# Performance work log

Measured on AMD Instinct MI355X. Metric: run time of the kernel, lower is better.

The kernel has to match this reference:

```python
import jax, jax.numpy as jnp
import numpy as np

C = 256  # num_channels
N = 524288  # number of 2D query points


def _linear_params(key, fan_in, fan_out):
    # torch nn.Linear default init: U(-1/sqrt(fan_in), 1/sqrt(fan_in))
    kw, kb = jax.random.split(key)
    bound = 1.0 / np.sqrt(fan_in)
    W = jax.random.uniform(kw, (fan_in, fan_out), jnp.float32, -bound, bound)
    b = jax.random.uniform(kb, (fan_out,), jnp.float32, -bound, bound)
    return W, b


def setup_inputs() -> dict:
    key = jax.random.key(0)
    k_uv, k0, k1, k2, k3 = jax.random.split(key, 5)
    uv = jax.random.uniform(k_uv, (N, 2), jnp.float32)
    W_in, b_in = _linear_params(k0, 4, C)
    W_h0, b_h0 = _linear_params(k1, C, C)
    W_h1, b_h1 = _linear_params(k2, C, C)
    W_out, b_out = _linear_params(k3, C, 3)
    return {
        "uv": uv,
        "W_in": W_in, "b_in": b_in,
        "W_h0": W_h0, "b_h0": b_h0,
        "W_h1": W_h1, "b_h1": b_h1,
        "W_out": W_out, "b_out": b_out,
    }


def reference(uv, W_in, b_in, W_h0, b_h0, W_h1, b_h1, W_out, b_out):
    # NOTE: in the original, `encoded = 2*pi*uv` is overwritten, so the
    # effective encoding is simply [cos(uv), sin(uv)] -> last dim 4.
    encoded = jnp.concatenate([jnp.cos(uv), jnp.sin(uv)], axis=-1)  # [N, 4]
    h = jax.nn.relu(encoded @ W_in + b_in)   # [N, C]
    h = jax.nn.relu(h @ W_h0 + b_h0)          # [N, C]
    h = jax.nn.relu(h @ W_h1 + b_h1)          # [N, C]
    out = jax.nn.sigmoid(h @ W_out + b_out)   # [N, 3]
    return out
```

## Files before the change

kernel.cpp:

```cpp
#include <hip/hip_runtime.h>
#include <hip/hip_bf16.h>
#include <math.h>

#define CCH 256
#define MT  64
#define ROWE 264
#define TPB 512

typedef __attribute__((ext_vector_type(8))) short short8;
typedef __attribute__((ext_vector_type(4))) float f32x4;
typedef __attribute__((ext_vector_type(2))) unsigned int uint2v;

__device__ unsigned short g_T0[CCH * CCH];
__device__ unsigned short g_T1[CCH * CCH];
__device__ unsigned short g_Wo[16 * CCH];

__device__ __forceinline__ unsigned short f2bf(float f) {
  unsigned u = __float_as_uint(f);
  u += 0x7fffu + ((u >> 16) & 1u);
  return (unsigned short)(u >> 16);
}
__device__ __forceinline__ unsigned cvtpk(float lo, float hi) {
  unsigned r;
  asm("v_cvt_pk_bf16_f32 %0, %1, %2" : "=v"(r) : "v"(lo), "v"(hi));
  return r;
}

__global__ void transpose_w(const float* __restrict__ W0,
                            const float* __restrict__ W1) {
  __shared__ float tile[32][33];
  const float* src = blockIdx.z ? W1 : W0;
  unsigned short* dst = blockIdx.z ? g_T1 : g_T0;
  const int tx = threadIdx.x, ty = threadIdx.y;
  const int k0 = blockIdx.y * 32, n0 = blockIdx.x * 32;
#pragma unroll
  for (int r = 0; r < 4; ++r)
    tile[ty + r * 8][tx] = src[(k0 + ty + r * 8) * CCH + n0 + tx];
  __syncthreads();
#pragma unroll
  for (int r = 0; r < 4; ++r) {
    const int n = n0 + ty + r * 8;
    dst[n * CCH + k0 + tx] = f2bf(tile[tx][ty + r * 8]);
  }
}

__global__ void prep_wo(const float* __restrict__ W_out) {
  const int k = threadIdx.x;
#pragma unroll
  for (int j = 0; j < 16; ++j)
    g_Wo[j * CCH + k] = (j < 3) ? f2bf(W_out[k * 3 + j]) : (unsigned short)0;
}

__device__ __forceinline__ void mfma_gemm(
    const unsigned short (*__restrict__ src)[ROWE],
    const unsigned short* __restrict__ Wt,
    f32x4 acc[4][2], int wv, int l16, int lk8) {
#pragma unroll
  for (int mt = 0; mt < 4; ++mt)
#pragma unroll
    for (int nt = 0; nt < 2; ++nt)
      acc[mt][nt] = (f32x4){0.f, 0.f, 0.f, 0.f};

  const unsigned short* w0p = &Wt[(wv * 32 + l16) * CCH + lk8 * 8];
  const unsigned short* w1p = w0p + 16 * CCH;
  const unsigned short* a0p = &src[l16][lk8 * 8];

#pragma unroll
  for (int kk = 0; kk < 8; ++kk) {
    const int k = kk * 32;
    const short8 w0 = *(const short8*)&w0p[k];
    const short8 w1 = *(const short8*)&w1p[k];
#pragma unroll
    for (int mt = 0; mt < 4; ++mt) {
      const short8 a = *(const short8*)&a0p[mt * 16 * ROWE + k];
      acc[mt][0] = __builtin_amdgcn_mfma_f32_16x16x32_bf16(w0, a, acc[mt][0], 0, 0, 0);
      acc[mt][1] = __builtin_amdgcn_mfma_f32_16x16x32_bf16(w1, a, acc[mt][1], 0, 0, 0);
    }
  }
}

__device__ __forceinline__ void epilogue_store(
    const f32x4 acc[4][2], unsigned short (*__restrict__ dst)[ROWE],
    const float* __restrict__ bias, int wv, int l16, int lk8) {
#pragma unroll
  for (int nt = 0; nt < 2; ++nt) {
    const int ch0 = wv * 32 + nt * 16 + lk8 * 4;
    const f32x4 bv = *(const f32x4*)&bias[ch0];
#pragma unroll
    for (int mt = 0; mt < 4; ++mt) {
      uint2v pk;
      pk[0] = cvtpk(fmaxf(acc[mt][nt][0] + bv[0], 0.f),
                    fmaxf(acc[mt][nt][1] + bv[1], 0.f));
      pk[1] = cvtpk(fmaxf(acc[mt][nt][2] + bv[2], 0.f),
                    fmaxf(acc[mt][nt][3] + bv[3], 0.f));
      *(uint2v*)&dst[mt * 16 + l16][ch0] = pk;
    }
  }
}

__global__ __launch_bounds__(TPB, 6) void nerf_fused(
    const float* __restrict__ uv,
    const float* __restrict__ W_in, const float* __restrict__ b_in,
    const float* __restrict__ b_h0, const float* __restrict__ b_h1,
    const float* __restrict__ b_out,
    float* __restrict__ out) {
  __shared__ unsigned short hA[MT][ROWE];

  const int tid = threadIdx.x;
  const long n0 = (long)blockIdx.x * MT;
  const int wv = tid >> 6, ln = tid & 63;
  const int l16 = ln & 15, lk8 = ln >> 4;

  {
    const int p = tid >> 3;
    const int t7 = tid & 7;
    const float u = uv[(n0 + p) * 2 + 0];
    const float v = uv[(n0 + p) * 2 + 1];
    const float e0 = __cosf(u), e1 = __cosf(v), e2 = __sinf(u), e3 = __sinf(v);
#pragma unroll
    for (int j = 0; j < 8; ++j) {
      const int c = t7 * 4 + j * 32;
      const f32x4 w0 = *(const f32x4*)&W_in[0 * CCH + c];
      const f32x4 w1 = *(const f32x4*)&W_in[1 * CCH + c];
      const f32x4 w2 = *(const f32x4*)&W_in[2 * CCH + c];
      const f32x4 w3 = *(const f32x4*)&W_in[3 * CCH + c];
      const f32x4 bb = *(const f32x4*)&b_in[c];
      float x[4];
#pragma unroll
      for (int i = 0; i < 4; ++i)
        x[i] = fmaxf(bb[i] + e0 * w0[i] + e1 * w1[i] + e2 * w2[i] + e3 * w3[i], 0.f);
      uint2v pk;
      pk[0] = cvtpk(x[0], x[1]);
      pk[1] = cvtpk(x[2], x[3]);
      *(uint2v*)&hA[p][c] = pk;
    }
  }
  __syncthreads();

  f32x4 acc[4][2];

  mfma_gemm(hA, g_T0, acc, wv, l16, lk8);
  __syncthreads();
  epilogue_store(acc, hA, b_h0, wv, l16, lk8);
  __syncthreads();

  mfma_gemm(hA, g_T1, acc, wv, l16, lk8);
  __syncthreads();
  epilogue_store(acc, hA, b_h1, wv, l16, lk8);
  __syncthreads();

  if (wv < 4) {
    f32x4 oacc = (f32x4){0.f, 0.f, 0.f, 0.f};
#pragma unroll
    for (int kk = 0; kk < 8; ++kk) {
      const int k = kk * 32 + lk8 * 8;
      const short8 wo = *(const short8*)&g_Wo[l16 * CCH + k];
      const short8 hb = *(const short8*)&hA[wv * 16 + l16][k];
      oacc = __builtin_amdgcn_mfma_f32_16x16x32_bf16(wo, hb, oacc, 0, 0, 0);
    }
    if (lk8 == 0) {
      const long pt = n0 + wv * 16 + l16;
#pragma unroll
      for (int i = 0; i < 3; ++i)
        out[pt * 3 + i] = 1.f / (1.f + __expf(-(oacc[i] + b_out[i])));
    }
  }
}

extern "C" void kernel_launch(void* const* d_in, const int* in_sizes, int n_in,
                              void* d_out, int out_size, void* d_ws, size_t ws_size,
                              hipStream_t stream) {
  const float* uv    = (const float*)d_in[0];
  const float* W_in  = (const float*)d_in[1];
  const float* b_in  = (const float*)d_in[2];
  const float* W_h0  = (const float*)d_in[3];
  const float* b_h0  = (const float*)d_in[4];
  const float* W_h1  = (const float*)d_in[5];
  const float* b_h1  = (const float*)d_in[6];
  const float* W_out = (const float*)d_in[7];
  const float* b_out = (const float*)d_in[8];

  const int N = in_sizes[0] / 2;

  transpose_w<<<dim3(8, 8, 2), dim3(32, 8), 0, stream>>>(W_h0, W_h1);
  prep_wo<<<1, CCH, 0, stream>>>(W_out);
  nerf_fused<<<dim3(N / MT), dim3(TPB), 0, stream>>>(
      uv, W_in, b_in, b_h0, b_h1, b_out, (float*)d_out);
}
```

Baseline: 417.9 us.

## Persistent kernel with LDS-resident weights and global h1 spill

Replaces the per-tile fused kernel with a persistent kernel of 256 blocks of 1024 threads, each handling 2048 points. Each weight matrix is loaded into LDS once per block, and the first layer's activations are computed in registers and fed straight into MFMA. The hidden state after layer 1 is spilled to a 256MB global bf16 buffer and re-read for layer 2, and the output layer becomes a scalar dot product with shuffle and LDS reduction. This removes the repeated global weight reads, but it adds a large round-trip of activations through global memory and a hardcoded N buffer, so the spill traffic may outweigh the weight reuse.

```diff
diff --git a/kernel.cpp b/kernel.cpp
--- a/kernel.cpp
+++ b/kernel.cpp
@@ -3,17 +3,23 @@
 #include <math.h>
 
 #define CCH 256
-#define MT  64
-#define ROWE 264
-#define TPB 512
+#define WROW 264
+#define TPB 1024
+#define NBLK 256
+#define PPB 2048
+#define PPI 256
+#define NITER 8
 
 typedef __attribute__((ext_vector_type(8))) short short8;
 typedef __attribute__((ext_vector_type(4))) float f32x4;
+typedef __attribute__((ext_vector_type(2))) float f32x2;
+typedef __attribute__((ext_vector_type(4))) unsigned int uint4v;
 typedef __attribute__((ext_vector_type(2))) unsigned int uint2v;
 
 __device__ unsigned short g_T0[CCH * CCH];
 __device__ unsigned short g_T1[CCH * CCH];
-__device__ unsigned short g_Wo[16 * CCH];
+__device__ float g_Wof[4 * CCH];
+__device__ unsigned short g_h1[(size_t)524288 * CCH];
 
 __device__ __forceinline__ unsigned short f2bf(float f) {
   unsigned u = __float_as_uint(f);
@@ -44,126 +50,180 @@
   }
 }
 
-__global__ void prep_wo(const float* __restrict__ W_out) {
+__global__ void prep_wof(const float* __restrict__ W_out) {
   const int k = threadIdx.x;
 #pragma unroll
-  for (int j = 0; j < 16; ++j)
-    g_Wo[j * CCH + k] = (j < 3) ? f2bf(W_out[k * 3 + j]) : (unsigned short)0;
-}
-
-__device__ __forceinline__ void mfma_gemm(
-    const unsigned short (*__restrict__ src)[ROWE],
-    const unsigned short* __restrict__ Wt,
-    f32x4 acc[4][2], int wv, int l16, int lk8) {
-#pragma unroll
-  for (int mt = 0; mt < 4; ++mt)
-#pragma unroll
-    for (int nt = 0; nt < 2; ++nt)
-      acc[mt][nt] = (f32x4){0.f, 0.f, 0.f, 0.f};
-
-  const unsigned short* w0p = &Wt[(wv * 32 + l16) * CCH + lk8 * 8];
-  const unsigned short* w1p = w0p + 16 * CCH;
-  const unsigned short* a0p = &src[l16][lk8 * 8];
-
-#pragma unroll
-  for (int kk = 0; kk < 8; ++kk) {
-    const int k = kk * 32;
-    const short8 w0 = *(const short8*)&w0p[k];
-    const short8 w1 = *(const short8*)&w1p[k];
-#pragma unroll
-    for (int mt = 0; mt < 4; ++mt) {
-      const short8 a = *(const short8*)&a0p[mt * 16 * ROWE + k];
-      acc[mt][0] = __builtin_amdgcn_mfma_f32_16x16x32_bf16(w0, a, acc[mt][0], 0, 0, 0);
-      acc[mt][1] = __builtin_amdgcn_mfma_f32_16x16x32_bf16(w1, a, acc[mt][1], 0, 0, 0);
-    }
-  }
-}
-
-__device__ __forceinline__ void epilogue_store(
-    const f32x4 acc[4][2], unsigned short (*__restrict__ dst)[ROWE],
-    const float* __restrict__ bias, int wv, int l16, int lk8) {
-#pragma unroll
-  for (int nt = 0; nt < 2; ++nt) {
-    const int ch0 = wv * 32 + nt * 16 + lk8 * 4;
-    const f32x4 bv = *(const f32x4*)&bias[ch0];
-#pragma unroll
-    for (int mt = 0; mt < 4; ++mt) {
-      uint2v pk;
-      pk[0] = cvtpk(fmaxf(acc[mt][nt][0] + bv[0], 0.f),
-                    fmaxf(acc[mt][nt][1] + bv[1], 0.f));
-      pk[1] = cvtpk(fmaxf(acc[mt][nt][2] + bv[2], 0.f),
-                    fmaxf(acc[mt][nt][3] + bv[3], 0.f));
-      *(uint2v*)&dst[mt * 16 + l16][ch0] = pk;
-    }
-  }
-}
-
-__global__ __launch_bounds__(TPB, 6) void nerf_fused(
+  for (int j = 0; j < 4; ++j)
+    g_Wof[j * CCH + k] = (j < 3) ? W_out[k * 3 + j] : 0.0f;
+}
+
+__global__ __launch_bounds__(TPB, 4) void nerf_persist(
     const float* __restrict__ uv,
     const float* __restrict__ W_in, const float* __restrict__ b_in,
     const float* __restrict__ b_h0, const float* __restrict__ b_h1,
     const float* __restrict__ b_out,
     float* __restrict__ out) {
-  __shared__ unsigned short hA[MT][ROWE];
+  __shared__ unsigned short Wlds[CCH][WROW];
+  __shared__ float scr[16][2][16][3];
 
   const int tid = threadIdx.x;
-  const long n0 = (long)blockIdx.x * MT;
   const int wv = tid >> 6, ln = tid & 63;
   const int l16 = ln & 15, lk8 = ln >> 4;
+  const int pg = wv >> 1;
+  const int chbase = (wv & 1) * 128;
+  const long blk0 = (long)blockIdx.x * PPB;
+  const float bo0 = b_out[0], bo1 = b_out[1], bo2 = b_out[2];
 
   {
-    const int p = tid >> 3;
-    const int t7 = tid & 7;
-    const float u = uv[(n0 + p) * 2 + 0];
-    const float v = uv[(n0 + p) * 2 + 1];
-    const float e0 = __cosf(u), e1 = __cosf(v), e2 = __sinf(u), e3 = __sinf(v);
-#pragma unroll
-    for (int j = 0; j < 8; ++j) {
-      const int c = t7 * 4 + j * 32;
-      const f32x4 w0 = *(const f32x4*)&W_in[0 * CCH + c];
-      const f32x4 w1 = *(const f32x4*)&W_in[1 * CCH + c];
-      const f32x4 w2 = *(const f32x4*)&W_in[2 * CCH + c];
-      const f32x4 w3 = *(const f32x4*)&W_in[3 * CCH + c];
-      const f32x4 bb = *(const f32x4*)&b_in[c];
-      float x[4];
-#pragma unroll
-      for (int i = 0; i < 4; ++i)
-        x[i] = fmaxf(bb[i] + e0 * w0[i] + e1 * w1[i] + e2 * w2[i] + e3 * w3[i], 0.f);
-      uint2v pk;
-      pk[0] = cvtpk(x[0], x[1]);
-      pk[1] = cvtpk(x[2], x[3]);
-      *(uint2v*)&hA[p][c] = pk;
-    }
-  }
-  __syncthreads();
-
-  f32x4 acc[4][2];
-
-  mfma_gemm(hA, g_T0, acc, wv, l16, lk8);
-  __syncthreads();
-  epilogue_store(acc, hA, b_h0, wv, l16, lk8);
-  __syncthreads();
-
-  mfma_gemm(hA, g_T1, acc, wv, l16, lk8);
-  __syncthreads();
-  epilogue_store(acc, hA, b_h1, wv, l16, lk8);
-  __syncthreads();
-
-  if (wv < 4) {
-    f32x4 oacc = (f32x4){0.f, 0.f, 0.f, 0.f};
+    const int r = tid >> 2, seg = tid & 3;
+    const uint4v* src = (const uint4v*)&g_T0[r * CCH + seg * 64];
+    uint4v* dst = (uint4v*)&Wlds[r][seg * 64];
+#pragma unroll
+    for (int j = 0; j < 8; ++j) dst[j] = src[j];
+  }
+  __syncthreads();
+
+  for (int it = 0; it < NITER; ++it) {
+    const long pt0 = blk0 + it * PPI + pg * 32 + l16;
+    const long pt1 = pt0 + 16;
+    const f32x2 uva = *(const f32x2*)&uv[pt0 * 2];
+    const f32x2 uvb = *(const f32x2*)&uv[pt1 * 2];
+    const float e0[4] = {__cosf(uva[0]), __cosf(uva[1]), __sinf(uva[0]), __sinf(uva[1])};
+    const float e1[4] = {__cosf(uvb[0]), __cosf(uvb[1]), __sinf(uvb[0]), __sinf(uvb[1])};
+
+    f32x4 acc[2][8];
+#pragma unroll
+    for (int mt = 0; mt < 2; ++mt)
+#pragma unroll
+      for (int nt = 0; nt < 8; ++nt)
+        acc[mt][nt] = (f32x4){0.f, 0.f, 0.f, 0.f};
+
 #pragma unroll
     for (int kk = 0; kk < 8; ++kk) {
-      const int k = kk * 32 + lk8 * 8;
-      const short8 wo = *(const short8*)&g_Wo[l16 * CCH + k];
-      const short8 hb = *(const short8*)&hA[wv * 16 + l16][k];
-      oacc = __builtin_amdgcn_mfma_f32_16x16x32_bf16(wo, hb, oacc, 0, 0, 0);
-    }
+      const int ch = kk * 32 + lk8 * 8;
+      uint4v p0, p1;
+#pragma unroll
+      for (int h = 0; h < 2; ++h) {
+        const int c4 = ch + h * 4;
+        const f32x4 w0 = *(const f32x4*)&W_in[0 * CCH + c4];
+        const f32x4 w1 = *(const f32x4*)&W_in[1 * CCH + c4];
+        const f32x4 w2 = *(const f32x4*)&W_in[2 * CCH + c4];
+        const f32x4 w3 = *(const f32x4*)&W_in[3 * CCH + c4];
+        const f32x4 bb = *(const f32x4*)&b_in[c4];
+        float x0[4], x1[4];
+#pragma unroll
+        for (int j = 0; j < 4; ++j) {
+          x0[j] = fmaxf(bb[j] + e0[0]*w0[j] + e0[1]*w1[j] + e0[2]*w2[j] + e0[3]*w3[j], 0.f);
+          x1[j] = fmaxf(bb[j] + e1[0]*w0[j] + e1[1]*w1[j] + e1[2]*w2[j] + e1[3]*w3[j], 0.f);
+        }
+        p0[h * 2 + 0] = cvtpk(x0[0], x0[1]); p0[h * 2 + 1] = cvtpk(x0[2], x0[3]);
+        p1[h * 2 + 0] = cvtpk(x1[0], x1[1]); p1[h * 2 + 1] = cvtpk(x1[2], x1[3]);
+      }
+      const short8 B0 = *(short8*)&p0;
+      const short8 B1 = *(short8*)&p1;
+#pragma unroll
+      for (int nt = 0; nt < 8; ++nt) {
+        const short8 A = *(const short8*)&Wlds[chbase + nt * 16 + l16][ch];
+        acc[0][nt] = __builtin_amdgcn_mfma_f32_16x16x32_bf16(A, B0, acc[0][nt], 0, 0, 0);
+        acc[1][nt] = __builtin_amdgcn_mfma_f32_16x16x32_bf16(A, B1, acc[1][nt], 0, 0, 0);
+      }
+    }
+#pragma unroll
+    for (int nt = 0; nt < 8; ++nt) {
+      const int ch0 = chbase + nt * 16 + lk8 * 4;
+      const f32x4 bv = *(const f32x4*)&b_h0[ch0];
+#pragma unroll
+      for (int mt = 0; mt < 2; ++mt) {
+        const long pt = mt ? pt1 : pt0;
+        uint2v pk;
+        pk[0] = cvtpk(fmaxf(acc[mt][nt][0] + bv[0], 0.f),
+                      fmaxf(acc[mt][nt][1] + bv[1], 0.f));
+        pk[1] = cvtpk(fmaxf(acc[mt][nt][2] + bv[2], 0.f),
+                      fmaxf(acc[mt][nt][3] + bv[3], 0.f));
+        *(uint2v*)&g_h1[pt * CCH + ch0] = pk;
+      }
+    }
+  }
+
+  __syncthreads();
+  {
+    const int r = tid >> 2, seg = tid & 3;
+    const uint4v* src = (const uint4v*)&g_T1[r * CCH + seg * 64];
+    uint4v* dst = (uint4v*)&Wlds[r][seg * 64];
+#pragma unroll
+    for (int j = 0; j < 8; ++j) dst[j] = src[j];
+  }
+  __syncthreads();
+
+  for (int it = 0; it < NITER; ++it) {
+    const long pt0 = blk0 + it * PPI + pg * 32 + l16;
+    const long pt1 = pt0 + 16;
+
+    f32x4 acc[2][8];
+#pragma unroll
+    for (int mt = 0; mt < 2; ++mt)
+#pragma unroll
+      for (int nt = 0; nt < 8; ++nt)
+        acc[mt][nt] = (f32x4){0.f, 0.f, 0.f, 0.f};
+
+#pragma unroll
+    for (int kk = 0; kk < 8; ++kk) {
+      const int ch = kk * 32 + lk8 * 8;
+      const short8 B0 = *(const short8*)&g_h1[pt0 * CCH + ch];
+      const short8 B1 = *(const short8*)&g_h1[pt1 * CCH + ch];
+#pragma unroll
+      for (int nt = 0; nt < 8; ++nt) {
+        const short8 A = *(const short8*)&Wlds[chbase + nt * 16 + l16][ch];
+        acc[0][nt] = __builtin_amdgcn_mfma_f32_16x16x32_bf16(A, B0, acc[0][nt], 0, 0, 0);
+        acc[1][nt] = __builtin_amdgcn_mfma_f32_16x16x32_bf16(A, B1, acc[1][nt], 0, 0, 0);
+      }
+    }
+
+    float s[2][3] = {{0.f, 0.f, 0.f}, {0.f, 0.f, 0.f}};
+#pragma unroll
+    for (int nt = 0; nt < 8; ++nt) {
+      const int ch0 = chbase + nt * 16 + lk8 * 4;
+      const f32x4 bv  = *(const f32x4*)&b_h1[ch0];
+      const f32x4 wo0 = *(const f32x4*)&g_Wof[0 * CCH + ch0];
+      const f32x4 wo1 = *(const f32x4*)&g_Wof[1 * CCH + ch0];
+      const f32x4 wo2 = *(const f32x4*)&g_Wof[2 * CCH + ch0];
+#pragma unroll
+      for (int mt = 0; mt < 2; ++mt)
+#pragma unroll
+        for (int i = 0; i < 4; ++i) {
+          const float h2 = fmaxf(acc[mt][nt][i] + bv[i], 0.f);
+          s[mt][0] += h2 * wo0[i];
+          s[mt][1] += h2 * wo1[i];
+          s[mt][2] += h2 * wo2[i];
+        }
+    }
+#pragma unroll
+    for (int mt = 0; mt < 2; ++mt)
+#pragma unroll
+      for (int j = 0; j < 3; ++j) {
+        s[mt][j] += __shfl_xor(s[mt][j], 16);
+        s[mt][j] += __shfl_xor(s[mt][j], 32);
+      }
     if (lk8 == 0) {
-      const long pt = n0 + wv * 16 + l16;
-#pragma unroll
-      for (int i = 0; i < 3; ++i)
-        out[pt * 3 + i] = 1.f / (1.f + __expf(-(oacc[i] + b_out[i])));
-    }
+#pragma unroll
+      for (int mt = 0; mt < 2; ++mt)
+#pragma unroll
+        for (int j = 0; j < 3; ++j) scr[wv][mt][l16][j] = s[mt][j];
+    }
+    __syncthreads();
+    if ((wv & 1) == 0 && lk8 == 0) {
+#pragma unroll
+      for (int mt = 0; mt < 2; ++mt) {
+        const long pt = mt ? pt1 : pt0;
+        const float t0 = scr[wv][mt][l16][0] + scr[wv + 1][mt][l16][0] + bo0;
+        const float t1 = scr[wv][mt][l16][1] + scr[wv + 1][mt][l16][1] + bo1;
+        const float t2 = scr[wv][mt][l16][2] + scr[wv + 1][mt][l16][2] + bo2;
+        out[pt * 3 + 0] = 1.f / (1.f + __expf(-t0));
+        out[pt * 3 + 1] = 1.f / (1.f + __expf(-t1));
+        out[pt * 3 + 2] = 1.f / (1.f + __expf(-t2));
+      }
+    }
+    __syncthreads();
   }
 }
 
@@ -180,10 +240,8 @@
   const float* W_out = (const float*)d_in[7];
   const float* b_out = (const float*)d_in[8];
 
-  const int N = in_sizes[0] / 2;
-
   transpose_w<<<dim3(8, 8, 2), dim3(32, 8), 0, stream>>>(W_h0, W_h1);
-  prep_wo<<<1, CCH, 0, stream>>>(W_out);
-  nerf_fused<<<dim3(N / MT), dim3(TPB), 0, stream>>>(
+  prep_wof<<<1, CCH, 0, stream>>>(W_out);
+  nerf_persist<<<dim3(NBLK), dim3(TPB), 0, stream>>>(
       uv, W_in, b_in, b_h0, b_h1, b_out, (float*)d_out);
 }
```

Measured after the change: 433.2 us. 3.7% more time.
